# Optimization experiments

Hardware: AMD Instinct MI355X
Metric: run time of the kernel (lower is better)

Reference implementation:

```python
import jax, jax.numpy as jnp
import numpy as np

MAX_LENGTH = 13
PAD_TOKEN = 0
HIDDEN = 1024
VOCAB = 32000
BATCH = 64


def gru_cell(x, h, w_ih, w_hh, b_ih, b_hh):
    # PyTorch GRU gate order: reset, update, new
    gi = x @ w_ih.T + b_ih            # [B, 3H]
    gh = h @ w_hh.T + b_hh            # [B, 3H]
    i_r, i_z, i_n = jnp.split(gi, 3, axis=-1)
    h_r, h_z, h_n = jnp.split(gh, 3, axis=-1)
    r = jax.nn.sigmoid(i_r + h_r)
    z = jax.nn.sigmoid(i_z + h_z)
    n = jnp.tanh(i_n + r * h_n)
    return (1.0 - z) * n + z * h


def setup_inputs() -> dict:
    key = jax.random.key(0)
    ks = jax.random.split(key, 9)
    s = 0.02
    return {
        "encoder_outputs": jax.random.normal(ks[0], (BATCH, MAX_LENGTH, HIDDEN), jnp.float32),
        "encoder_hidden": jax.random.normal(ks[1], (1, BATCH, HIDDEN), jnp.float32),
        "embedding": jax.random.normal(ks[2], (VOCAB, HIDDEN), jnp.float32) * s,
        "w_ih": jax.random.normal(ks[3], (3 * HIDDEN, HIDDEN), jnp.float32) * s,
        "w_hh": jax.random.normal(ks[4], (3 * HIDDEN, HIDDEN), jnp.float32) * s,
        "b_ih": jnp.zeros((3 * HIDDEN,), jnp.float32),
        "b_hh": jnp.zeros((3 * HIDDEN,), jnp.float32),
        "w_out": jax.random.normal(ks[5], (VOCAB, HIDDEN), jnp.float32) * s,
        "b_out": jnp.zeros((VOCAB,), jnp.float32),
    }


def reference(encoder_outputs, encoder_hidden, embedding, w_ih, w_hh, b_ih, b_hh, w_out, b_out):
    batch = encoder_outputs.shape[0]
    h0 = encoder_hidden[0]                               # [B, H]
    tok0 = jnp.full((batch,), PAD_TOKEN, dtype=jnp.int32)

    def step(carry, _):
        h, tok = carry
        x = jax.nn.relu(embedding[tok])                  # embed + relu
        h = gru_cell(x, h, w_ih, w_hh, b_ih, b_hh)       # GRU cell
        logits = h @ w_out.T + b_out                     # [B, V]
        nxt = jnp.argmax(logits, axis=-1).astype(jnp.int32)  # greedy feedback (topk(1))
        return (h, nxt), logits

    (h_final, _), logits = jax.lax.scan(step, (h0, tok0), None, length=MAX_LENGTH)
    logits = jnp.transpose(logits, (1, 0, 2))            # [B, T, V]
    log_probs = jax.nn.log_softmax(logits, axis=-1)
    return log_probs, h_final[None]
```

## Files before the change

kernel.cpp:

```cpp
#include <hip/hip_runtime.h>
#include <math.h>

#define BB 64
#define HH 1024
#define VV 32000
#define TT 13
#define QS 8000
#define BKL 128

typedef float f32x4 __attribute__((ext_vector_type(4)));
typedef __bf16 bf16x8 __attribute__((ext_vector_type(8)));

__device__ __forceinline__ unsigned short f2bf(float f) {
  unsigned u = __float_as_uint(f);
  u = (u + 0x7fffu + ((u >> 16) & 1u)) >> 16;
  return (unsigned short)u;
}
__device__ __forceinline__ float bf2f(unsigned short s) {
  return __uint_as_float(((unsigned)s) << 16);
}

__device__ __forceinline__ void gld16(const void* g, void* l) {
  __builtin_amdgcn_global_load_lds(
      (const __attribute__((address_space(1))) unsigned int*)g,
      (__attribute__((address_space(3))) unsigned int*)l, 16, 0, 0);
}

__global__ __launch_bounds__(1024) void k_init(
    const float* __restrict__ enc, const float* __restrict__ emb,
    float* __restrict__ hrm, unsigned short* __restrict__ hhi,
    unsigned short* __restrict__ hlo, unsigned short* __restrict__ xhi,
    unsigned short* __restrict__ xlo) {
  const int g = blockIdx.x * 1024 + threadIdx.x;
  const float h = enc[g];
  hrm[g] = h;
  const unsigned short h16 = f2bf(h);
  hhi[g] = h16;
  hlo[g] = f2bf(h - bf2f(h16));
  float e = emb[threadIdx.x];
  e = e > 0.f ? e : 0.f;
  const unsigned short e16 = f2bf(e);
  xhi[g] = e16;
  xlo[g] = f2bf(e - bf2f(e16));
}

__global__ __launch_bounds__(256) void k_wconv(const float* __restrict__ w,
                                               unsigned short* __restrict__ o) {
  const int n4 = VV * HH / 4;
  for (int i = blockIdx.x * 256 + threadIdx.x; i < n4; i += gridDim.x * 256) {
    const f32x4 v = ((const f32x4*)w)[i];
    ushort4 u;
    u.x = f2bf(v[0]); u.y = f2bf(v[1]); u.z = f2bf(v[2]); u.w = f2bf(v[3]);
    ((ushort4*)o)[i] = u;
  }
}

__global__ __launch_bounds__(256) void k_wconv2(
    const float* __restrict__ wih, const float* __restrict__ whh,
    unsigned short* __restrict__ ghi, unsigned short* __restrict__ glo) {
  const int n4 = 6 * HH * HH / 4;
  for (int i = blockIdx.x * 256 + threadIdx.x; i < n4; i += gridDim.x * 256) {
    const int flat = i * 4;
    const float* src = flat < 3 * HH * HH ? wih + flat : whh + (flat - 3 * HH * HH);
    const f32x4 v = *(const f32x4*)src;
    ushort4 hi, lo;
    hi.x = f2bf(v[0]); lo.x = f2bf(v[0] - bf2f(hi.x));
    hi.y = f2bf(v[1]); lo.y = f2bf(v[1] - bf2f(hi.y));
    hi.z = f2bf(v[2]); lo.z = f2bf(v[2] - bf2f(hi.z));
    hi.w = f2bf(v[3]); lo.w = f2bf(v[3] - bf2f(hi.w));
    ((ushort4*)ghi)[i] = hi;
    ((ushort4*)glo)[i] = lo;
  }
}

__global__ __launch_bounds__(64) void k_gru(
    const unsigned short* __restrict__ xhi, const unsigned short* __restrict__ xlo,
    const unsigned short* __restrict__ hhi_s, const unsigned short* __restrict__ hlo_s,
    const unsigned short* __restrict__ ghi, const unsigned short* __restrict__ glo,
    const float* __restrict__ wih, const float* __restrict__ whh,
    float* __restrict__ gbuf, int cachegw) {
  const int blk = blockIdx.x, lane = threadIdx.x;
  const int kh = blk & 1;
  const int r2 = blk >> 1;
  const int g6 = r2 % 6, jt = r2 / 6;
  const unsigned short* Ahi = g6 < 3 ? xhi : hhi_s;
  const unsigned short* Alo = g6 < 3 ? xlo : hlo_s;
  const int cl = lane & 15, kk = (lane >> 4) * 8;
  const int j = jt * 16 + cl;
  const int kbeg = kh * 512;
  f32x4 acc[4];
  acc[0] = acc[1] = acc[2] = acc[3] = (f32x4){0.f, 0.f, 0.f, 0.f};

  if (cachegw) {
    const unsigned short* bh = ghi + (size_t)(g6 * HH + j) * HH + kbeg;
    const unsigned short* bl = glo + (size_t)(g6 * HH + j) * HH + kbeg;
    const unsigned short* ah = Ahi + kbeg;
    const unsigned short* al = Alo + kbeg;
    #pragma unroll 4
    for (int k0 = 0; k0 < 512; k0 += 32) {
      const bf16x8 whi = *(const bf16x8*)(bh + k0 + kk);
      const bf16x8 wlo = *(const bf16x8*)(bl + k0 + kk);
      #pragma unroll
      for (int rt = 0; rt < 4; ++rt) {
        const size_t aoff = (size_t)(rt * 16 + cl) * HH + k0 + kk;
        const bf16x8 a_h = *(const bf16x8*)(ah + aoff);
        const bf16x8 a_l = *(const bf16x8*)(al + aoff);
        acc[rt] = __builtin_amdgcn_mfma_f32_16x16x32_bf16(a_h, whi, acc[rt], 0, 0, 0);
        acc[rt] = __builtin_amdgcn_mfma_f32_16x16x32_bf16(a_l, whi, acc[rt], 0, 0, 0);
        acc[rt] = __builtin_amdgcn_mfma_f32_16x16x32_bf16(a_h, wlo, acc[rt], 0, 0, 0);
      }
    }
  } else {
    const float* W = (g6 < 3 ? wih : whh) + (size_t)((g6 % 3) * HH + j) * HH + kbeg;
    for (int k0 = 0; k0 < 512; k0 += 32) {
      const f32x4 w0 = *(const f32x4*)(W + k0 + kk);
      const f32x4 w1 = *(const f32x4*)(W + k0 + kk + 4);
      union { unsigned short u[8]; bf16x8 b; } chi, clo;
      #pragma unroll
      for (int u2 = 0; u2 < 4; ++u2) {
        chi.u[u2] = f2bf(w0[u2]); clo.u[u2] = f2bf(w0[u2] - bf2f(chi.u[u2]));
        chi.u[4 + u2] = f2bf(w1[u2]); clo.u[4 + u2] = f2bf(w1[u2] - bf2f(chi.u[4 + u2]));
      }
      #pragma unroll
      for (int rt = 0; rt < 4; ++rt) {
        const size_t aoff = (size_t)(rt * 16 + cl) * HH + kbeg + k0 + kk;
        const bf16x8 a_h = *(const bf16x8*)(Ahi + aoff);
        const bf16x8 a_l = *(const bf16x8*)(Alo + aoff);
        acc[rt] = __builtin_amdgcn_mfma_f32_16x16x32_bf16(a_h, chi.b, acc[rt], 0, 0, 0);
        acc[rt] = __builtin_amdgcn_mfma_f32_16x16x32_bf16(a_l, chi.b, acc[rt], 0, 0, 0);
        acc[rt] = __builtin_amdgcn_mfma_f32_16x16x32_bf16(a_h, clo.b, acc[rt], 0, 0, 0);
      }
    }
  }
  #pragma unroll
  for (int rt = 0; rt < 4; ++rt)
    #pragma unroll
    for (int rg = 0; rg < 4; ++rg) {
      const int row = rt * 16 + (lane >> 4) * 4 + rg;
      gbuf[(size_t)((kh * 6 + g6) * BB + row) * HH + jt * 16 + cl] = acc[rt][rg];
    }
}

__global__ __launch_bounds__(256) void k_gep(
    const float* __restrict__ gbuf, const float* __restrict__ bih,
    const float* __restrict__ bhh, const float* __restrict__ hsrc,
    float* __restrict__ hdst, unsigned short* __restrict__ hhi_d,
    unsigned short* __restrict__ hlo_d) {
  const int e = blockIdx.x * 256 + threadIdx.x;
  const int b = e >> 10, j = e & (HH - 1);
  const size_t base = (size_t)b * HH + j;
  const float gir = gbuf[(size_t)(0 * BB + b) * HH + j] + gbuf[(size_t)((6 + 0) * BB + b) * HH + j] + bih[j];
  const float giz = gbuf[(size_t)(1 * BB + b) * HH + j] + gbuf[(size_t)((6 + 1) * BB + b) * HH + j] + bih[HH + j];
  const float gin = gbuf[(size_t)(2 * BB + b) * HH + j] + gbuf[(size_t)((6 + 2) * BB + b) * HH + j] + bih[2 * HH + j];
  const float ghr = gbuf[(size_t)(3 * BB + b) * HH + j] + gbuf[(size_t)((6 + 3) * BB + b) * HH + j] + bhh[j];
  const float ghz = gbuf[(size_t)(4 * BB + b) * HH + j] + gbuf[(size_t)((6 + 4) * BB + b) * HH + j] + bhh[HH + j];
  const float ghn = gbuf[(size_t)(5 * BB + b) * HH + j] + gbuf[(size_t)((6 + 5) * BB + b) * HH + j] + bhh[2 * HH + j];
  const float r_ = 1.f / (1.f + __expf(-(gir + ghr)));
  const float z_ = 1.f / (1.f + __expf(-(giz + ghz)));
  const float n_ = tanhf(gin + r_ * ghn);
  const float hnew = (1.f - z_) * n_ + z_ * hsrc[base];
  hdst[base] = hnew;
  const unsigned short h16 = f2bf(hnew);
  hhi_d[base] = h16;
  hlo_d[base] = f2bf(hnew - bf2f(h16));
}

__global__ __launch_bounds__(512, 1) void k_logits_lds(
    const unsigned short* __restrict__ hb,
    const unsigned short* __restrict__ wbf,
    const float* __restrict__ bout, float* __restrict__ lbuf) {
  __shared__ __attribute__((aligned(16))) unsigned char sA[2][64 * BKL * 2];
  __shared__ __attribute__((aligned(16))) unsigned char sB[2][128 * BKL * 2];
  const int tid = threadIdx.x, blk = blockIdx.x;
  const int lane = tid & 63, wv = tid >> 6;
  const int cl = lane & 15, kk = (lane >> 4) * 8;

  auto STAGE = [&](int buf, int k0) {
    #pragma unroll
    for (int it = 0; it < 2; ++it) {
      const int c = it * 512 + tid;
      const int r = c >> 4;
      const int kb = (c & 15) * 16;
      const int kbs = kb ^ ((r & 7) << 4);
      gld16(hb + (size_t)r * HH + k0 + (kbs >> 1),
            &sA[buf][it * 8192 + wv * 1024]);
    }
    #pragma unroll
    for (int it = 0; it < 4; ++it) {
      const int c = it * 512 + tid;
      const int col = c >> 4;
      const int kb = (c & 15) * 16;
      const int kbs = kb ^ ((col & 7) << 4);
      gld16(wbf + (size_t)(blk * 128 + col) * HH + k0 + (kbs >> 1),
            &sB[buf][it * 8192 + wv * 1024]);
    }
  };

  f32x4 acc[4];
  acc[0] = acc[1] = acc[2] = acc[3] = (f32x4){0.f, 0.f, 0.f, 0.f};

  STAGE(0, 0);
  for (int t = 0; t < HH / BKL; ++t) {
    const int cur = t & 1;
    if (t < HH / BKL - 1) {
      STAGE(cur ^ 1, (t + 1) * BKL);
      asm volatile("s_waitcnt vmcnt(6)" ::: "memory");
    } else {
      asm volatile("s_waitcnt vmcnt(0)" ::: "memory");
    }
    __builtin_amdgcn_s_barrier();
    __builtin_amdgcn_sched_barrier(0);
    #pragma unroll
    for (int ks = 0; ks < BKL; ks += 32) {
      const int bc = wv * 16 + cl;
      const bf16x8 bfr = *(const bf16x8*)&sB[cur][bc * (BKL * 2) + (((ks + kk) * 2) ^ ((bc & 7) << 4))];
      #pragma unroll
      for (int rt = 0; rt < 4; ++rt) {
        const int ar = rt * 16 + cl;
        const bf16x8 afr = *(const bf16x8*)&sA[cur][ar * (BKL * 2) + (((ks + kk) * 2) ^ ((ar & 7) << 4))];
        acc[rt] = __builtin_amdgcn_mfma_f32_16x16x32_bf16(afr, bfr, acc[rt], 0, 0, 0);
      }
    }
    __builtin_amdgcn_s_barrier();
    __builtin_amdgcn_sched_barrier(0);
  }

  const int col = blk * 128 + wv * 16 + cl;
  const float bo = bout[col];
  #pragma unroll
  for (int rt = 0; rt < 4; ++rt)
    #pragma unroll
    for (int rg = 0; rg < 4; ++rg) {
      const int row = rt * 16 + (lane >> 4) * 4 + rg;
      lbuf[(size_t)row * VV + col] = acc[rt][rg] + bo;
    }
}

__global__ __launch_bounds__(256) void k_logits_fb(
    const unsigned short* __restrict__ hb, const float* __restrict__ wout,
    const float* __restrict__ bout, float* __restrict__ lbuf) {
  const int tid = threadIdx.x, blk = blockIdx.x;
  const int lane = tid & 63, wv = tid >> 6;
  const int n0 = blk * 64 + wv * 16;
  const int cl = lane & 15, kk = (lane >> 4) * 8;
  f32x4 acc[4];
  acc[0] = acc[1] = acc[2] = acc[3] = (f32x4){0.f, 0.f, 0.f, 0.f};
  const float* wrow = wout + (size_t)(n0 + cl) * HH;
  for (int k0 = 0; k0 < HH; k0 += 32) {
    const f32x4 w0 = *(const f32x4*)(wrow + k0 + kk);
    const f32x4 w1 = *(const f32x4*)(wrow + k0 + kk + 4);
    union { unsigned short u[8]; bf16x8 b; } cv;
    #pragma unroll
    for (int u2 = 0; u2 < 4; ++u2) { cv.u[u2] = f2bf(w0[u2]); cv.u[4 + u2] = f2bf(w1[u2]); }
    #pragma unroll
    for (int rt = 0; rt < 4; ++rt) {
      const bf16x8 afr = *(const bf16x8*)(hb + (size_t)(rt * 16 + cl) * HH + k0 + kk);
      acc[rt] = __builtin_amdgcn_mfma_f32_16x16x32_bf16(afr, cv.b, acc[rt], 0, 0, 0);
    }
  }
  const int col = n0 + cl;
  const float bo = bout[col];
  #pragma unroll
  for (int rt = 0; rt < 4; ++rt)
    #pragma unroll
    for (int rg = 0; rg < 4; ++rg) {
      const int row = rt * 16 + (lane >> 4) * 4 + rg;
      lbuf[(size_t)row * VV + col] = acc[rt][rg] + bo;
    }
}

__global__ __launch_bounds__(256) void k_sum(
    const float* __restrict__ lbuf, const float* __restrict__ wout,
    const float* __restrict__ bout, const float* __restrict__ hnew,
    float* __restrict__ mq, float* __restrict__ sq,
    float* __restrict__ qbestV, int* __restrict__ qbestI, int dorecheck) {
  __shared__ float srow[QS];
  __shared__ float red[4];
  __shared__ int icnt;
  __shared__ int scand[32];
  const int tid = threadIdx.x;
  const int b = blockIdx.x >> 2, q = blockIdx.x & 3;
  const int lane = tid & 63, wv = tid >> 6;
  const f32x4* src = (const f32x4*)(lbuf + (size_t)b * VV + q * QS);
  f32x4* s4 = (f32x4*)srow;

  float m = -3.0e38f;
  for (int i = tid; i < QS / 4; i += 256) {
    const f32x4 v = src[i];
    s4[i] = v;
    m = fmaxf(fmaxf(fmaxf(m, v[0]), v[1]), fmaxf(v[2], v[3]));
  }
  #pragma unroll
  for (int d = 1; d < 64; d <<= 1) m = fmaxf(m, __shfl_xor(m, d, 64));
  if (lane == 0) red[wv] = m;
  if (tid == 0) icnt = 0;
  __syncthreads();
  const float M = fmaxf(fmaxf(red[0], red[1]), fmaxf(red[2], red[3]));

  float s = 0.f;
  for (int i = tid; i < QS / 4; i += 256) {
    const f32x4 v = s4[i];
    s += __expf(v[0] - M) + __expf(v[1] - M) + __expf(v[2] - M) + __expf(v[3] - M);
  }
  #pragma unroll
  for (int d = 1; d < 64; d <<= 1) s += __shfl_xor(s, d, 64);
  __syncthreads();
  if (lane == 0) red[wv] = s;
  __syncthreads();
  if (tid == 0) {
    mq[b * 4 + q] = M;
    sq[b * 4 + q] = red[0] + red[1] + red[2] + red[3];
  }

  if (dorecheck) {
    const float thr = M - 0.05f;
    for (int i = tid; i < QS / 4; i += 256) {
      const f32x4 v = s4[i];
      #pragma unroll
      for (int u = 0; u < 4; ++u)
        if (v[u] >= thr) {
          const int c = atomicAdd(&icnt, 1);
          if (c < 32) scand[c] = q * QS + 4 * i + u;
        }
    }
    __syncthreads();
    if (wv == 0) {
      const int nc = icnt < 32 ? icnt : 32;
      const float* hrow = hnew + (size_t)b * HH;
      f32x4 h4[4];
      #pragma unroll
      for (int u = 0; u < 4; ++u) h4[u] = *(const f32x4*)(hrow + lane * 16 + u * 4);
      float best = -3.0e38f; int bi = 0x7fffffff;
      for (int ci = 0; ci < nc; ++ci) {
        const int v = scand[ci];
        const float* wrow = wout + (size_t)v * HH + lane * 16;
        float ss = 0.f;
        #pragma unroll
        for (int u = 0; u < 4; ++u) {
          const f32x4 w4 = *(const f32x4*)(wrow + u * 4);
          ss += h4[u][0] * w4[0] + h4[u][1] * w4[1] + h4[u][2] * w4[2] + h4[u][3] * w4[3];
        }
        #pragma unroll
        for (int d = 1; d < 64; d <<= 1) ss += __shfl_xor(ss, d, 64);
        ss += bout[v];
        if (ss > best || (ss == best && v < bi)) { best = ss; bi = v; }
      }
      if (lane == 0) { qbestV[b * 4 + q] = best; qbestI[b * 4 + q] = bi; }
    }
  }
}

__global__ __launch_bounds__(256) void k_out(
    const float* __restrict__ lbuf, const float* __restrict__ mq,
    const float* __restrict__ sq, const float* __restrict__ qbestV,
    const int* __restrict__ qbestI, const float* __restrict__ emb,
    const float* __restrict__ hnew, float* __restrict__ out,
    unsigned short* __restrict__ xhi, unsigned short* __restrict__ xlo, int t) {
  __shared__ int stok;
  const int tid = threadIdx.x;
  const int b = blockIdx.x >> 2, q = blockIdx.x & 3;

  const float m0 = mq[b * 4 + 0], m1 = mq[b * 4 + 1];
  const float m2 = mq[b * 4 + 2], m3 = mq[b * 4 + 3];
  const float Mg = fmaxf(fmaxf(m0, m1), fmaxf(m2, m3));
  const float Sg = sq[b * 4 + 0] * __expf(m0 - Mg) + sq[b * 4 + 1] * __expf(m1 - Mg) +
                   sq[b * 4 + 2] * __expf(m2 - Mg) + sq[b * 4 + 3] * __expf(m3 - Mg);
  const float LZ = Mg + logf(Sg);

  const f32x4* src = (const f32x4*)(lbuf + (size_t)b * VV + q * QS);
  f32x4* dst = (f32x4*)(out + ((size_t)b * TT + t) * VV + q * QS);
  for (int i = tid; i < QS / 4; i += 256)
    dst[i] = src[i] - LZ;

  if (q == 0 && t < TT - 1) {
    if (tid == 0) {
      float bv = qbestV[b * 4 + 0]; int bi = qbestI[b * 4 + 0];
      #pragma unroll
      for (int qq = 1; qq < 4; ++qq) {
        const float v = qbestV[b * 4 + qq]; const int i2 = qbestI[b * 4 + qq];
        if (v > bv || (v == bv && i2 < bi)) { bv = v; bi = i2; }
      }
      stok = bi;
    }
    __syncthreads();
    const int tok = stok;
    for (int j = tid; j < HH; j += 256) {
      float e = emb[(size_t)tok * HH + j];
      e = e > 0.f ? e : 0.f;
      const unsigned short e16 = f2bf(e);
      xhi[(size_t)b * HH + j] = e16;
      xlo[(size_t)b * HH + j] = f2bf(e - bf2f(e16));
    }
  }
  if (q == 0 && t == TT - 1) {
    for (int j = tid; j < HH; j += 256)
      out[(size_t)BB * TT * VV + (size_t)b * HH + j] = hnew[(size_t)b * HH + j];
  }
}

extern "C" void kernel_launch(void* const* d_in, const int* in_sizes, int n_in,
                              void* d_out, int out_size, void* d_ws, size_t ws_size,
                              hipStream_t stream) {
  const float* enc  = (const float*)d_in[1];
  const float* emb  = (const float*)d_in[2];
  const float* wih  = (const float*)d_in[3];
  const float* whh  = (const float*)d_in[4];
  const float* bih  = (const float*)d_in[5];
  const float* bhh  = (const float*)d_in[6];
  const float* wout = (const float*)d_in[7];
  const float* bout = (const float*)d_in[8];
  float* out = (float*)d_out;

  char* ws = (char*)d_ws;
  size_t off = 0;
  auto alloc = [&](size_t bytes) -> char* {
    char* p = ws + off;
    off += (bytes + 255) & ~(size_t)255;
    return p;
  };
  float* hrm = (float*)alloc((size_t)2 * BB * HH * 4);
  unsigned short* hhi = (unsigned short*)alloc((size_t)2 * BB * HH * 2);
  unsigned short* hlo = (unsigned short*)alloc((size_t)2 * BB * HH * 2);
  unsigned short* xhi = (unsigned short*)alloc((size_t)BB * HH * 2);
  unsigned short* xlo = (unsigned short*)alloc((size_t)BB * HH * 2);
  float* gbuf = (float*)alloc((size_t)12 * BB * HH * 4);
  float* lbuf = (float*)alloc((size_t)BB * VV * 4);
  float* mq = (float*)alloc((size_t)BB * 4 * 4);
  float* sq = (float*)alloc((size_t)BB * 4 * 4);
  float* qbestV = (float*)alloc((size_t)BB * 4 * 4);
  int* qbestI = (int*)alloc((size_t)BB * 4 * 4);
  unsigned short* wbf = (unsigned short*)alloc((size_t)VV * HH * 2);
  const int cachew = (ws_size >= off) ? 1 : 0;
  unsigned short* ghi = (unsigned short*)alloc((size_t)6 * HH * HH * 2);
  unsigned short* glo = (unsigned short*)alloc((size_t)6 * HH * HH * 2);
  const int cachegw = (ws_size >= off) ? 1 : 0;

  hipLaunchKernelGGL(k_init, dim3(64), dim3(1024), 0, stream,
                     enc, emb, hrm, hhi, hlo, xhi, xlo);
  if (cachew)
    hipLaunchKernelGGL(k_wconv, dim3(2048), dim3(256), 0, stream, wout, wbf);
  if (cachegw)
    hipLaunchKernelGGL(k_wconv2, dim3(1024), dim3(256), 0, stream, wih, whh, ghi, glo);

  for (int t = 0; t < TT; ++t) {
    const int p = t & 1;
    const float* hsrc = hrm + (size_t)p * BB * HH;
    float* hdst = hrm + (size_t)(p ^ 1) * BB * HH;
    const unsigned short* hhs = hhi + (size_t)p * BB * HH;
    const unsigned short* hls = hlo + (size_t)p * BB * HH;
    unsigned short* hhd = hhi + (size_t)(p ^ 1) * BB * HH;
    unsigned short* hld = hlo + (size_t)(p ^ 1) * BB * HH;

    hipLaunchKernelGGL(k_gru, dim3(768), dim3(64), 0, stream,
                       xhi, xlo, hhs, hls, ghi, glo, wih, whh, gbuf, cachegw);
    hipLaunchKernelGGL(k_gep, dim3(256), dim3(256), 0, stream,
                       gbuf, bih, bhh, hsrc, hdst, hhd, hld);
    if (cachew)
      hipLaunchKernelGGL(k_logits_lds, dim3(250), dim3(512), 0, stream,
                         hhd, wbf, bout, lbuf);
    else
      hipLaunchKernelGGL(k_logits_fb, dim3(500), dim3(256), 0, stream,
                         hhd, wout, bout, lbuf);
    hipLaunchKernelGGL(k_sum, dim3(256), dim3(256), 0, stream,
                       lbuf, wout, bout, hdst, mq, sq, qbestV, qbestI,
                       (t < TT - 1) ? 1 : 0);
    hipLaunchKernelGGL(k_out, dim3(256), dim3(256), 0, stream,
                       lbuf, mq, sq, qbestV, qbestI, emb, hdst, out, xhi, xlo, t);
  }
}
```

Measured before the change: 927.0 us.

## Fuse decode loop into persistent megakernel with software grid barriers

Replaces the 5 kernel launches per timestep with a single persistent kernel of 256 blocks that runs all 13 steps. Steps are separated by an atomic-counter grid barrier. The GRU gate GEMM and the elementwise gate math are fused per block through shared memory, which removes the gbuf round-trip. Each block's logits slice is kept in LDS between the softmax reduction and the output write. This targets launch overhead and global-memory traffic, but it depends on all 256 blocks being co-resident for the spin barrier and gives the GRU GEMM less parallelism (one block per 4 columns).

```diff
diff --git a/kernel.cpp b/kernel.cpp
--- a/kernel.cpp
+++ b/kernel.cpp
@@ -7,6 +7,8 @@
 #define TT 13
 #define QS 8000
 #define BKL 128
+#define MB 256
+#define MT 512
 
 typedef float f32x4 __attribute__((ext_vector_type(4)));
 typedef __bf16 bf16x8 __attribute__((ext_vector_type(8)));
@@ -26,11 +28,26 @@
       (__attribute__((address_space(3))) unsigned int*)l, 16, 0, 0);
 }
 
+__device__ __forceinline__ void gsync(unsigned* bar, unsigned target) {
+  __syncthreads();
+  if (threadIdx.x == 0) {
+    __hip_atomic_fetch_add(bar, 1u, __ATOMIC_RELEASE, __HIP_MEMORY_SCOPE_AGENT);
+    int spins = 0;
+    while (__hip_atomic_load(bar, __ATOMIC_RELAXED, __HIP_MEMORY_SCOPE_AGENT) < target) {
+      __builtin_amdgcn_s_sleep(2);
+      if (((++spins) & 1023) == 0)
+        (void)__hip_atomic_load(bar, __ATOMIC_ACQUIRE, __HIP_MEMORY_SCOPE_AGENT);
+    }
+    (void)__hip_atomic_load(bar, __ATOMIC_ACQUIRE, __HIP_MEMORY_SCOPE_AGENT);
+  }
+  __syncthreads();
+}
+
 __global__ __launch_bounds__(1024) void k_init(
     const float* __restrict__ enc, const float* __restrict__ emb,
     float* __restrict__ hrm, unsigned short* __restrict__ hhi,
     unsigned short* __restrict__ hlo, unsigned short* __restrict__ xhi,
-    unsigned short* __restrict__ xlo) {
+    unsigned short* __restrict__ xlo, unsigned* __restrict__ bar) {
   const int g = blockIdx.x * 1024 + threadIdx.x;
   const float h = enc[g];
   hrm[g] = h;
@@ -42,6 +59,7 @@
   const unsigned short e16 = f2bf(e);
   xhi[g] = e16;
   xlo[g] = f2bf(e - bf2f(e16));
+  if (blockIdx.x == 0 && threadIdx.x < 16) bar[threadIdx.x] = 0u;
 }
 
 __global__ __launch_bounds__(256) void k_wconv(const float* __restrict__ w,
@@ -73,12 +91,270 @@
   }
 }
 
-__global__ __launch_bounds__(64) void k_gru(
+__global__ __launch_bounds__(512, 1) void k_mega(
+    const float* emb, const float* wout, const float* bout,
+    const float* bih, const float* bhh,
+    const unsigned short* ghi, const unsigned short* glo,
+    const unsigned short* wbf,
+    float* hrm, unsigned short* hhi, unsigned short* hlo,
+    unsigned short* xhi, unsigned short* xlo,
+    float* lbuf, float* mq, float* sq, float* qbestV, int* qbestI,
+    float* out, unsigned* bar) {
+  __shared__ __attribute__((aligned(16))) union {
+    struct { unsigned char A[2][64 * BKL * 2]; unsigned char B[2][128 * BKL * 2]; } lg;
+    struct { float srow[QS]; float red[8]; int icnt; int stok; int scand[32]; } sm;
+    struct { float g[6][64][9]; } gr;
+  } u;
+  const int blk = blockIdx.x, tid = threadIdx.x;
+  const int lane = tid & 63, wv = tid >> 6;
+  const int cl = lane & 15, kk = (lane >> 4) * 8;
+  unsigned barNo = 0;
+
+  for (int t = 0; t < TT; ++t) {
+    const int p = t & 1;
+    const float* hsrc = hrm + (size_t)p * BB * HH;
+    float* hdst = hrm + (size_t)(p ^ 1) * BB * HH;
+    const unsigned short* hhs = hhi + (size_t)p * BB * HH;
+    const unsigned short* hls = hlo + (size_t)p * BB * HH;
+    unsigned short* hhd = hhi + (size_t)(p ^ 1) * BB * HH;
+    unsigned short* hld = hlo + (size_t)(p ^ 1) * BB * HH;
+
+    if (wv < 6) {
+      const int g6 = wv;
+      const unsigned short* Ahi = g6 < 3 ? xhi : hhs;
+      const unsigned short* Alo = g6 < 3 ? xlo : hls;
+      const int col = blk * 4 + (cl & 3);
+      const unsigned short* bh = ghi + (size_t)(g6 * HH + col) * HH;
+      const unsigned short* bl = glo + (size_t)(g6 * HH + col) * HH;
+      f32x4 acc[4];
+      acc[0] = acc[1] = acc[2] = acc[3] = (f32x4){0.f, 0.f, 0.f, 0.f};
+      #pragma unroll 4
+      for (int k0 = 0; k0 < HH; k0 += 32) {
+        const bf16x8 whi = *(const bf16x8*)(bh + k0 + kk);
+        const bf16x8 wlo = *(const bf16x8*)(bl + k0 + kk);
+        #pragma unroll
+        for (int rt = 0; rt < 4; ++rt) {
+          const size_t aoff = (size_t)(rt * 16 + cl) * HH + k0 + kk;
+          const bf16x8 a_h = *(const bf16x8*)(Ahi + aoff);
+          const bf16x8 a_l = *(const bf16x8*)(Alo + aoff);
+          acc[rt] = __builtin_amdgcn_mfma_f32_16x16x32_bf16(a_h, whi, acc[rt], 0, 0, 0);
+          acc[rt] = __builtin_amdgcn_mfma_f32_16x16x32_bf16(a_l, whi, acc[rt], 0, 0, 0);
+          acc[rt] = __builtin_amdgcn_mfma_f32_16x16x32_bf16(a_h, wlo, acc[rt], 0, 0, 0);
+        }
+      }
+      if (cl < 4) {
+        #pragma unroll
+        for (int rt = 0; rt < 4; ++rt)
+          #pragma unroll
+          for (int rg = 0; rg < 4; ++rg)
+            u.gr.g[g6][rt * 16 + (lane >> 4) * 4 + rg][cl] = acc[rt][rg];
+      }
+    }
+    __syncthreads();
+    if (tid < 256) {
+      const int c = tid & 3, b = tid >> 2;
+      const int j = blk * 4 + c;
+      const size_t base = (size_t)b * HH + j;
+      const float gir = u.gr.g[0][b][c] + bih[j];
+      const float giz = u.gr.g[1][b][c] + bih[HH + j];
+      const float gin = u.gr.g[2][b][c] + bih[2 * HH + j];
+      const float ghr = u.gr.g[3][b][c] + bhh[j];
+      const float ghz = u.gr.g[4][b][c] + bhh[HH + j];
+      const float ghn = u.gr.g[5][b][c] + bhh[2 * HH + j];
+      const float r_ = 1.f / (1.f + __expf(-(gir + ghr)));
+      const float z_ = 1.f / (1.f + __expf(-(giz + ghz)));
+      const float n_ = tanhf(gin + r_ * ghn);
+      const float hnew = (1.f - z_) * n_ + z_ * hsrc[base];
+      hdst[base] = hnew;
+      const unsigned short h16 = f2bf(hnew);
+      hhd[base] = h16;
+      hld[base] = f2bf(hnew - bf2f(h16));
+    }
+    gsync(bar, ++barNo * MB);
+
+    if (blk < 250) {
+      auto STAGE = [&](int buf, int k0) {
+        #pragma unroll
+        for (int it = 0; it < 2; ++it) {
+          const int c = it * 512 + tid;
+          const int r = c >> 4;
+          const int kb = (c & 15) * 16;
+          const int kbs = kb ^ ((r & 7) << 4);
+          gld16(hhd + (size_t)r * HH + k0 + (kbs >> 1),
+                &u.lg.A[buf][it * 8192 + wv * 1024]);
+        }
+        #pragma unroll
+        for (int it = 0; it < 4; ++it) {
+          const int c = it * 512 + tid;
+          const int col = c >> 4;
+          const int kb = (c & 15) * 16;
+          const int kbs = kb ^ ((col & 7) << 4);
+          gld16(wbf + (size_t)(blk * 128 + col) * HH + k0 + (kbs >> 1),
+                &u.lg.B[buf][it * 8192 + wv * 1024]);
+        }
+      };
+      f32x4 acc[4];
+      acc[0] = acc[1] = acc[2] = acc[3] = (f32x4){0.f, 0.f, 0.f, 0.f};
+      STAGE(0, 0);
+      for (int kt = 0; kt < HH / BKL; ++kt) {
+        const int cur = kt & 1;
+        if (kt < HH / BKL - 1) {
+          STAGE(cur ^ 1, (kt + 1) * BKL);
+          asm volatile("s_waitcnt vmcnt(6)" ::: "memory");
+        } else {
+          asm volatile("s_waitcnt vmcnt(0)" ::: "memory");
+        }
+        __builtin_amdgcn_s_barrier();
+        __builtin_amdgcn_sched_barrier(0);
+        #pragma unroll
+        for (int ks = 0; ks < BKL; ks += 32) {
+          const int bc = wv * 16 + cl;
+          const bf16x8 bfr = *(const bf16x8*)&u.lg.B[cur][bc * (BKL * 2) + (((ks + kk) * 2) ^ ((bc & 7) << 4))];
+          #pragma unroll
+          for (int rt = 0; rt < 4; ++rt) {
+            const int ar = rt * 16 + cl;
+            const bf16x8 afr = *(const bf16x8*)&u.lg.A[cur][ar * (BKL * 2) + (((ks + kk) * 2) ^ ((ar & 7) << 4))];
+            acc[rt] = __builtin_amdgcn_mfma_f32_16x16x32_bf16(afr, bfr, acc[rt], 0, 0, 0);
+          }
+        }
+        __builtin_amdgcn_s_barrier();
+        __builtin_amdgcn_sched_barrier(0);
+      }
+      const int col = blk * 128 + wv * 16 + cl;
+      const float bo = bout[col];
+      #pragma unroll
+      for (int rt = 0; rt < 4; ++rt)
+        #pragma unroll
+        for (int rg = 0; rg < 4; ++rg) {
+          const int row = rt * 16 + (lane >> 4) * 4 + rg;
+          lbuf[(size_t)row * VV + col] = acc[rt][rg] + bo;
+        }
+    }
+    gsync(bar, ++barNo * MB);
+
+    {
+      const int b = blk >> 2, q = blk & 3;
+      const f32x4* src = (const f32x4*)(lbuf + (size_t)b * VV + q * QS);
+      f32x4* s4 = (f32x4*)u.sm.srow;
+      float m = -3.0e38f;
+      for (int i = tid; i < QS / 4; i += MT) {
+        const f32x4 v = src[i];
+        s4[i] = v;
+        m = fmaxf(fmaxf(fmaxf(m, v[0]), v[1]), fmaxf(v[2], v[3]));
+      }
+      #pragma unroll
+      for (int d = 1; d < 64; d <<= 1) m = fmaxf(m, __shfl_xor(m, d, 64));
+      if (lane == 0) u.sm.red[wv] = m;
+      if (tid == 0) u.sm.icnt = 0;
+      __syncthreads();
+      float M = u.sm.red[0];
+      #pragma unroll
+      for (int w = 1; w < 8; ++w) M = fmaxf(M, u.sm.red[w]);
+
+      float s = 0.f;
+      for (int i = tid; i < QS / 4; i += MT) {
+        const f32x4 v = s4[i];
+        s += __expf(v[0] - M) + __expf(v[1] - M) + __expf(v[2] - M) + __expf(v[3] - M);
+      }
+      #pragma unroll
+      for (int d = 1; d < 64; d <<= 1) s += __shfl_xor(s, d, 64);
+      __syncthreads();
+      if (lane == 0) u.sm.red[wv] = s;
+      __syncthreads();
+      if (tid == 0) {
+        float S = 0.f;
+        #pragma unroll
+        for (int w = 0; w < 8; ++w) S += u.sm.red[w];
+        mq[b * 4 + q] = M;
+        sq[b * 4 + q] = S;
+      }
+      if (t < TT - 1) {
+        const float thr = M - 0.05f;
+        for (int i = tid; i < QS / 4; i += MT) {
+          const f32x4 v = s4[i];
+          #pragma unroll
+          for (int uu = 0; uu < 4; ++uu)
+            if (v[uu] >= thr) {
+              const int c = atomicAdd(&u.sm.icnt, 1);
+              if (c < 32) u.sm.scand[c] = q * QS + 4 * i + uu;
+            }
+        }
+        __syncthreads();
+        if (wv == 0) {
+          const int nc = u.sm.icnt < 32 ? u.sm.icnt : 32;
+          const float* hrow = hdst + (size_t)b * HH;
+          f32x4 h4[4];
+          #pragma unroll
+          for (int uu = 0; uu < 4; ++uu) h4[uu] = *(const f32x4*)(hrow + lane * 16 + uu * 4);
+          float best = -3.0e38f; int bi = 0x7fffffff;
+          for (int ci = 0; ci < nc; ++ci) {
+            const int v = u.sm.scand[ci];
+            const float* wrow = wout + (size_t)v * HH + lane * 16;
+            float ss = 0.f;
+            #pragma unroll
+            for (int uu = 0; uu < 4; ++uu) {
+              const f32x4 w4 = *(const f32x4*)(wrow + uu * 4);
+              ss += h4[uu][0] * w4[0] + h4[uu][1] * w4[1] + h4[uu][2] * w4[2] + h4[uu][3] * w4[3];
+            }
+            #pragma unroll
+            for (int d = 1; d < 64; d <<= 1) ss += __shfl_xor(ss, d, 64);
+            ss += bout[v];
+            if (ss > best || (ss == best && v < bi)) { best = ss; bi = v; }
+          }
+          if (lane == 0) { qbestV[b * 4 + q] = best; qbestI[b * 4 + q] = bi; }
+        }
+      }
+    }
+    gsync(bar, ++barNo * MB);
+
+    {
+      const int b = blk >> 2, q = blk & 3;
+      const float m0 = mq[b * 4 + 0], m1 = mq[b * 4 + 1];
+      const float m2 = mq[b * 4 + 2], m3 = mq[b * 4 + 3];
+      const float Mg = fmaxf(fmaxf(m0, m1), fmaxf(m2, m3));
+      const float Sg = sq[b * 4 + 0] * __expf(m0 - Mg) + sq[b * 4 + 1] * __expf(m1 - Mg) +
+                       sq[b * 4 + 2] * __expf(m2 - Mg) + sq[b * 4 + 3] * __expf(m3 - Mg);
+      const float LZ = Mg + logf(Sg);
+
+      const f32x4* s4 = (const f32x4*)u.sm.srow;
+      f32x4* dst = (f32x4*)(out + ((size_t)b * TT + t) * VV + q * QS);
+      for (int i = tid; i < QS / 4; i += MT)
+        dst[i] = s4[i] - LZ;
+
+      if (q == 0 && t < TT - 1) {
+        if (tid == 0) {
+          float bv = qbestV[b * 4 + 0]; int bi = qbestI[b * 4 + 0];
+          #pragma unroll
+          for (int qq = 1; qq < 4; ++qq) {
+            const float v = qbestV[b * 4 + qq]; const int i2 = qbestI[b * 4 + qq];
+            if (v > bv || (v == bv && i2 < bi)) { bv = v; bi = i2; }
+          }
+          u.sm.stok = bi;
+        }
+        __syncthreads();
+        const int tok = u.sm.stok;
+        for (int j = tid; j < HH; j += MT) {
+          float e = emb[(size_t)tok * HH + j];
+          e = e > 0.f ? e : 0.f;
+          const unsigned short e16 = f2bf(e);
+          xhi[(size_t)b * HH + j] = e16;
+          xlo[(size_t)b * HH + j] = f2bf(e - bf2f(e16));
+        }
+      }
+      if (q == 0 && t == TT - 1) {
+        for (int j = tid; j < HH; j += MT)
+          out[(size_t)BB * TT * VV + (size_t)b * HH + j] = hdst[(size_t)b * HH + j];
+      }
+    }
+    if (t < TT - 1) gsync(bar, ++barNo * MB);
+  }
+}
+
+__global__ __launch_bounds__(64) void k_gru_fb(
     const unsigned short* __restrict__ xhi, const unsigned short* __restrict__ xlo,
     const unsigned short* __restrict__ hhi_s, const unsigned short* __restrict__ hlo_s,
-    const unsigned short* __restrict__ ghi, const unsigned short* __restrict__ glo,
     const float* __restrict__ wih, const float* __restrict__ whh,
-    float* __restrict__ gbuf, int cachegw) {
+    float* __restrict__ gbuf) {
   const int blk = blockIdx.x, lane = threadIdx.x;
   const int kh = blk & 1;
   const int r2 = blk >> 1;
@@ -90,46 +366,24 @@
   const int kbeg = kh * 512;
   f32x4 acc[4];
   acc[0] = acc[1] = acc[2] = acc[3] = (f32x4){0.f, 0.f, 0.f, 0.f};
-
-  if (cachegw) {
-    const unsigned short* bh = ghi + (size_t)(g6 * HH + j) * HH + kbeg;
-    const unsigned short* bl = glo + (size_t)(g6 * HH + j) * HH + kbeg;
-    const unsigned short* ah = Ahi + kbeg;
-    const unsigned short* al = Alo + kbeg;
-    #pragma unroll 4
-    for (int k0 = 0; k0 < 512; k0 += 32) {
-      const bf16x8 whi = *(const bf16x8*)(bh + k0 + kk);
-      const bf16x8 wlo = *(const bf16x8*)(bl + k0 + kk);
-      #pragma unroll
-      for (int rt = 0; rt < 4; ++rt) {
-        const size_t aoff = (size_t)(rt * 16 + cl) * HH + k0 + kk;
-        const bf16x8 a_h = *(const bf16x8*)(ah + aoff);
-        const bf16x8 a_l = *(const bf16x8*)(al + aoff);
-        acc[rt] = __builtin_amdgcn_mfma_f32_16x16x32_bf16(a_h, whi, acc[rt], 0, 0, 0);
-        acc[rt] = __builtin_amdgcn_mfma_f32_16x16x32_bf16(a_l, whi, acc[rt], 0, 0, 0);
-        acc[rt] = __builtin_amdgcn_mfma_f32_16x16x32_bf16(a_h, wlo, acc[rt], 0, 0, 0);
-      }
-    }
-  } else {
-    const float* W = (g6 < 3 ? wih : whh) + (size_t)((g6 % 3) * HH + j) * HH + kbeg;
-    for (int k0 = 0; k0 < 512; k0 += 32) {
-      const f32x4 w0 = *(const f32x4*)(W + k0 + kk);
-      const f32x4 w1 = *(const f32x4*)(W + k0 + kk + 4);
-      union { unsigned short u[8]; bf16x8 b; } chi, clo;
-      #pragma unroll
-      for (int u2 = 0; u2 < 4; ++u2) {
-        chi.u[u2] = f2bf(w0[u2]); clo.u[u2] = f2bf(w0[u2] - bf2f(chi.u[u2]));
-        chi.u[4 + u2] = f2bf(w1[u2]); clo.u[4 + u2] = f2bf(w1[u2] - bf2f(chi.u[4 + u2]));
-      }
-      #pragma unroll
-      for (int rt = 0; rt < 4; ++rt) {
-        const size_t aoff = (size_t)(rt * 16 + cl) * HH + kbeg + k0 + kk;
-        const bf16x8 a_h = *(const bf16x8*)(Ahi + aoff);
-        const bf16x8 a_l = *(const bf16x8*)(Alo + aoff);
-        acc[rt] = __builtin_amdgcn_mfma_f32_16x16x32_bf16(a_h, chi.b, acc[rt], 0, 0, 0);
-        acc[rt] = __builtin_amdgcn_mfma_f32_16x16x32_bf16(a_l, chi.b, acc[rt], 0, 0, 0);
-        acc[rt] = __builtin_amdgcn_mfma_f32_16x16x32_bf16(a_h, clo.b, acc[rt], 0, 0, 0);
-      }
+  const float* W = (g6 < 3 ? wih : whh) + (size_t)((g6 % 3) * HH + j) * HH + kbeg;
+  for (int k0 = 0; k0 < 512; k0 += 32) {
+    const f32x4 w0 = *(const f32x4*)(W + k0 + kk);
+    const f32x4 w1 = *(const f32x4*)(W + k0 + kk + 4);
+    union { unsigned short u[8]; bf16x8 b; } chi, clo;
+    #pragma unroll
+    for (int u2 = 0; u2 < 4; ++u2) {
+      chi.u[u2] = f2bf(w0[u2]); clo.u[u2] = f2bf(w0[u2] - bf2f(chi.u[u2]));
+      chi.u[4 + u2] = f2bf(w1[u2]); clo.u[4 + u2] = f2bf(w1[u2] - bf2f(chi.u[4 + u2]));
+    }
+    #pragma unroll
+    for (int rt = 0; rt < 4; ++rt) {
+      const size_t aoff = (size_t)(rt * 16 + cl) * HH + kbeg + k0 + kk;
+      const bf16x8 a_h = *(const bf16x8*)(Ahi + aoff);
+      const bf16x8 a_l = *(const bf16x8*)(Alo + aoff);
+      acc[rt] = __builtin_amdgcn_mfma_f32_16x16x32_bf16(a_h, chi.b, acc[rt], 0, 0, 0);
+      acc[rt] = __builtin_amdgcn_mfma_f32_16x16x32_bf16(a_l, chi.b, acc[rt], 0, 0, 0);
+      acc[rt] = __builtin_amdgcn_mfma_f32_16x16x32_bf16(a_h, clo.b, acc[rt], 0, 0, 0);
     }
   }
   #pragma unroll
@@ -165,77 +419,6 @@
   hlo_d[base] = f2bf(hnew - bf2f(h16));
 }
 
-__global__ __launch_bounds__(512, 1) void k_logits_lds(
-    const unsigned short* __restrict__ hb,
-    const unsigned short* __restrict__ wbf,
-    const float* __restrict__ bout, float* __restrict__ lbuf) {
-  __shared__ __attribute__((aligned(16))) unsigned char sA[2][64 * BKL * 2];
-  __shared__ __attribute__((aligned(16))) unsigned char sB[2][128 * BKL * 2];
-  const int tid = threadIdx.x, blk = blockIdx.x;
-  const int lane = tid & 63, wv = tid >> 6;
-  const int cl = lane & 15, kk = (lane >> 4) * 8;
-
-  auto STAGE = [&](int buf, int k0) {
-    #pragma unroll
-    for (int it = 0; it < 2; ++it) {
-      const int c = it * 512 + tid;
-      const int r = c >> 4;
-      const int kb = (c & 15) * 16;
-      const int kbs = kb ^ ((r & 7) << 4);
-      gld16(hb + (size_t)r * HH + k0 + (kbs >> 1),
-            &sA[buf][it * 8192 + wv * 1024]);
-    }
-    #pragma unroll
-    for (int it = 0; it < 4; ++it) {
-      const int c = it * 512 + tid;
-      const int col = c >> 4;
-      const int kb = (c & 15) * 16;
-      const int kbs = kb ^ ((col & 7) << 4);
-      gld16(wbf + (size_t)(blk * 128 + col) * HH + k0 + (kbs >> 1),
-            &sB[buf][it * 8192 + wv * 1024]);
-    }
-  };
-
-  f32x4 acc[4];
-  acc[0] = acc[1] = acc[2] = acc[3] = (f32x4){0.f, 0.f, 0.f, 0.f};
-
-  STAGE(0, 0);
-  for (int t = 0; t < HH / BKL; ++t) {
-    const int cur = t & 1;
-    if (t < HH / BKL - 1) {
-      STAGE(cur ^ 1, (t + 1) * BKL);
-      asm volatile("s_waitcnt vmcnt(6)" ::: "memory");
-    } else {
-      asm volatile("s_waitcnt vmcnt(0)" ::: "memory");
-    }
-    __builtin_amdgcn_s_barrier();
-    __builtin_amdgcn_sched_barrier(0);
-    #pragma unroll
-    for (int ks = 0; ks < BKL; ks += 32) {
-      const int bc = wv * 16 + cl;
-      const bf16x8 bfr = *(const bf16x8*)&sB[cur][bc * (BKL * 2) + (((ks + kk) * 2) ^ ((bc & 7) << 4))];
-      #pragma unroll
-      for (int rt = 0; rt < 4; ++rt) {
-        const int ar = rt * 16 + cl;
-        const bf16x8 afr = *(const bf16x8*)&sA[cur][ar * (BKL * 2) + (((ks + kk) * 2) ^ ((ar & 7) << 4))];
-        acc[rt] = __builtin_amdgcn_mfma_f32_16x16x32_bf16(afr, bfr, acc[rt], 0, 0, 0);
-      }
-    }
-    __builtin_amdgcn_s_barrier();
-    __builtin_amdgcn_sched_barrier(0);
-  }
-
-  const int col = blk * 128 + wv * 16 + cl;
-  const float bo = bout[col];
-  #pragma unroll
-  for (int rt = 0; rt < 4; ++rt)
-    #pragma unroll
-    for (int rg = 0; rg < 4; ++rg) {
-      const int row = rt * 16 + (lane >> 4) * 4 + rg;
-      lbuf[(size_t)row * VV + col] = acc[rt][rg] + bo;
-    }
-}
-
 __global__ __launch_bounds__(256) void k_logits_fb(
     const unsigned short* __restrict__ hb, const float* __restrict__ wout,
     const float* __restrict__ bout, float* __restrict__ lbuf) {
@@ -269,7 +452,7 @@
     }
 }
 
-__global__ __launch_bounds__(256) void k_sum(
+__global__ __launch_bounds__(256) void k_sum_fb(
     const float* __restrict__ lbuf, const float* __restrict__ wout,
     const float* __restrict__ bout, const float* __restrict__ hnew,
     float* __restrict__ mq, float* __restrict__ sq,
@@ -283,7 +466,6 @@
   const int lane = tid & 63, wv = tid >> 6;
   const f32x4* src = (const f32x4*)(lbuf + (size_t)b * VV + q * QS);
   f32x4* s4 = (f32x4*)srow;
-
   float m = -3.0e38f;
   for (int i = tid; i < QS / 4; i += 256) {
     const f32x4 v = src[i];
@@ -296,7 +478,6 @@
   if (tid == 0) icnt = 0;
   __syncthreads();
   const float M = fmaxf(fmaxf(red[0], red[1]), fmaxf(red[2], red[3]));
-
   float s = 0.f;
   for (int i = tid; i < QS / 4; i += 256) {
     const f32x4 v = s4[i];
@@ -311,7 +492,6 @@
     mq[b * 4 + q] = M;
     sq[b * 4 + q] = red[0] + red[1] + red[2] + red[3];
   }
-
   if (dorecheck) {
     const float thr = M - 0.05f;
     for (int i = tid; i < QS / 4; i += 256) {
@@ -350,7 +530,7 @@
   }
 }
 
-__global__ __launch_bounds__(256) void k_out(
+__global__ __launch_bounds__(256) void k_out_fb(
     const float* __restrict__ lbuf, const float* __restrict__ mq,
     const float* __restrict__ sq, const float* __restrict__ qbestV,
     const int* __restrict__ qbestI, const float* __restrict__ emb,
@@ -359,19 +539,16 @@
   __shared__ int stok;
   const int tid = threadIdx.x;
   const int b = blockIdx.x >> 2, q = blockIdx.x & 3;
-
   const float m0 = mq[b * 4 + 0], m1 = mq[b * 4 + 1];
   const float m2 = mq[b * 4 + 2], m3 = mq[b * 4 + 3];
   const float Mg = fmaxf(fmaxf(m0, m1), fmaxf(m2, m3));
   const float Sg = sq[b * 4 + 0] * __expf(m0 - Mg) + sq[b * 4 + 1] * __expf(m1 - Mg) +
                    sq[b * 4 + 2] * __expf(m2 - Mg) + sq[b * 4 + 3] * __expf(m3 - Mg);
   const float LZ = Mg + logf(Sg);
-
   const f32x4* src = (const f32x4*)(lbuf + (size_t)b * VV + q * QS);
   f32x4* dst = (f32x4*)(out + ((size_t)b * TT + t) * VV + q * QS);
   for (int i = tid; i < QS / 4; i += 256)
     dst[i] = src[i] - LZ;
-
   if (q == 0 && t < TT - 1) {
     if (tid == 0) {
       float bv = qbestV[b * 4 + 0]; int bi = qbestI[b * 4 + 0];
@@ -429,42 +606,42 @@
   float* sq = (float*)alloc((size_t)BB * 4 * 4);
   float* qbestV = (float*)alloc((size_t)BB * 4 * 4);
   int* qbestI = (int*)alloc((size_t)BB * 4 * 4);
+  unsigned* bar = (unsigned*)alloc(64 * 4);
   unsigned short* wbf = (unsigned short*)alloc((size_t)VV * HH * 2);
-  const int cachew = (ws_size >= off) ? 1 : 0;
   unsigned short* ghi = (unsigned short*)alloc((size_t)6 * HH * HH * 2);
   unsigned short* glo = (unsigned short*)alloc((size_t)6 * HH * HH * 2);
-  const int cachegw = (ws_size >= off) ? 1 : 0;
+  const int cache_ok = (ws_size >= off) ? 1 : 0;
 
   hipLaunchKernelGGL(k_init, dim3(64), dim3(1024), 0, stream,
-                     enc, emb, hrm, hhi, hlo, xhi, xlo);
-  if (cachew)
+                     enc, emb, hrm, hhi, hlo, xhi, xlo, bar);
+
+  if (cache_ok) {
     hipLaunchKernelGGL(k_wconv, dim3(2048), dim3(256), 0, stream, wout, wbf);
-  if (cachegw)
     hipLaunchKernelGGL(k_wconv2, dim3(1024), dim3(256), 0, stream, wih, whh, ghi, glo);
-
-  for (int t = 0; t < TT; ++t) {
-    const int p = t & 1;
-    const float* hsrc = hrm + (size_t)p * BB * HH;
-    float* hdst = hrm + (size_t)(p ^ 1) * BB * HH;
-    const unsigned short* hhs = hhi + (size_t)p * BB * HH;
-    const unsigned short* hls = hlo + (size_t)p * BB * HH;
-    unsigned short* hhd = hhi + (size_t)(p ^ 1) * BB * HH;
-    unsigned short* hld = hlo + (size_t)(p ^ 1) * BB * HH;
-
-    hipLaunchKernelGGL(k_gru, dim3(768), dim3(64), 0, stream,
-                       xhi, xlo, hhs, hls, ghi, glo, wih, whh, gbuf, cachegw);
-    hipLaunchKernelGGL(k_gep, dim3(256), dim3(256), 0, stream,
-                       gbuf, bih, bhh, hsrc, hdst, hhd, hld);
-    if (cachew)
-      hipLaunchKernelGGL(k_logits_lds, dim3(250), dim3(512), 0, stream,
-                         hhd, wbf, bout, lbuf);
-    else
+    hipLaunchKernelGGL(k_mega, dim3(MB), dim3(MT), 0, stream,
+                       emb, wout, bout, bih, bhh, ghi, glo, wbf,
+                       hrm, hhi, hlo, xhi, xlo,
+                       lbuf, mq, sq, qbestV, qbestI, out, bar);
+  } else {
+    for (int t = 0; t < TT; ++t) {
+      const int p = t & 1;
+      const float* hsrc = hrm + (size_t)p * BB * HH;
+      float* hdst = hrm + (size_t)(p ^ 1) * BB * HH;
+      const unsigned short* hhs = hhi + (size_t)p * BB * HH;
+      const unsigned short* hls = hlo + (size_t)p * BB * HH;
+      unsigned short* hhd = hhi + (size_t)(p ^ 1) * BB * HH;
+      unsigned short* hld = hlo + (size_t)(p ^ 1) * BB * HH;
+      hipLaunchKernelGGL(k_gru_fb, dim3(768), dim3(64), 0, stream,
+                         xhi, xlo, hhs, hls, wih, whh, gbuf);
+      hipLaunchKernelGGL(k_gep, dim3(256), dim3(256), 0, stream,
+                         gbuf, bih, bhh, hsrc, hdst, hhd, hld);
       hipLaunchKernelGGL(k_logits_fb, dim3(500), dim3(256), 0, stream,
                          hhd, wout, bout, lbuf);
-    hipLaunchKernelGGL(k_sum, dim3(256), dim3(256), 0, stream,
-                       lbuf, wout, bout, hdst, mq, sq, qbestV, qbestI,
-                       (t < TT - 1) ? 1 : 0);
-    hipLaunchKernelGGL(k_out, dim3(256), dim3(256), 0, stream,
-                       lbuf, mq, sq, qbestV, qbestI, emb, hdst, out, xhi, xlo, t);
-  }
-}
+      hipLaunchKernelGGL(k_sum_fb, dim3(256), dim3(256), 0, stream,
+                         lbuf, wout, bout, hdst, mq, sq, qbestV, qbestI,
+                         (t < TT - 1) ? 1 : 0);
+      hipLaunchKernelGGL(k_out_fb, dim3(256), dim3(256), 0, stream,
+                         lbuf, mq, sq, qbestV, qbestI, emb, hdst, out, xhi, xlo, t);
+    }
+  }
+}
```

Measured after the change: 2.286 ms. 147% more time.
